# Kernel optimization log

Measured on AMD Instinct MI355X. Metric: run time of the kernel, lower is better.

The kernel has to match this reference:

```python
import jax, jax.numpy as jnp
import numpy as np

DEPTH = 6
IN_DIM = 768
NODE_HIDDEN = 16
LEAF_HIDDEN = 128
OUT_DIM = 768
BATCH = 4096
N_NODES = 2 ** DEPTH - 1   # 63 gating MLPs (heap/BFS order, root first)
N_LEAVES = 2 ** DEPTH      # 64 leaf MLPs


def setup_inputs() -> dict:
    key = jax.random.key(0)
    ks = jax.random.split(key, 5)
    def winit(k, shape, fan_in):
        return jax.random.normal(k, shape, jnp.float32) * (1.0 / np.sqrt(fan_in))
    return {
        "x": jax.random.normal(ks[0], (BATCH, IN_DIM), jnp.float32),
        "node_w1": winit(ks[1], (N_NODES, IN_DIM, NODE_HIDDEN), IN_DIM),
        "node_b1": jnp.zeros((N_NODES, NODE_HIDDEN), jnp.float32),
        "node_w2": winit(ks[2], (N_NODES, NODE_HIDDEN, 1), NODE_HIDDEN),
        "node_b2": jnp.zeros((N_NODES, 1), jnp.float32),
        "leaf_w1": winit(ks[3], (N_LEAVES, IN_DIM, LEAF_HIDDEN), IN_DIM),
        "leaf_b1": jnp.zeros((N_LEAVES, LEAF_HIDDEN), jnp.float32),
        "leaf_w2": winit(ks[4], (N_LEAVES, LEAF_HIDDEN, OUT_DIM), LEAF_HIDDEN),
        "leaf_b2": jnp.zeros((N_LEAVES, OUT_DIM), jnp.float32),
    }


def reference(x, node_w1, node_b1, node_w2, node_b2,
              leaf_w1, leaf_b1, leaf_w2, leaf_b2):
    """Training-mode (soft-gating) FFF tree, fully batched over all nodes/leaves.

    Equivalent to the recursive torch forward with training=True and the
    stochastic output-swap disabled (swap is a training-noise trick).
    """
    B = x.shape[0]
    # All node gates in one pass: c[b, n] = sigmoid(W2 @ relu(W1 @ x + b1) + b2)
    hn = jax.nn.relu(jnp.einsum('bi,nih->bnh', x, node_w1) + node_b1)
    c = jax.nn.sigmoid(jnp.einsum('bnh,nho->bno', hn, node_w2) + node_b2)[..., 0]  # [B, N_NODES]
    # All leaf MLPs in one pass (identity out activation)
    hl = jax.nn.relu(jnp.einsum('bi,lih->blh', x, leaf_w1) + leaf_b1)             # [B, L, LEAF_HIDDEN]
    y = jnp.einsum('blh,lho->blo', hl, leaf_w2) + leaf_b2                         # [B, L, OUT]
    # Leaf mixture weights: product of c (left) / (1-c) (right) along root->leaf path.
    # Heap index idx has children 2*idx, 2*idx+1; gate c weights the LEFT child.
    w = jnp.ones((B, 1), x.dtype)
    for lvl in range(DEPTH):
        g = c[:, 2 ** lvl - 1: 2 ** (lvl + 1) - 1]        # gates at this level, [B, 2^lvl]
        w = jnp.stack([w * g, w * (1.0 - g)], axis=-1).reshape(B, 2 ** (lvl + 1))
    return jnp.einsum('bl,blo->bo', w, y)                 # [B, OUT]
```

## Files before the change

kernel.cpp:

```cpp
#include <hip/hip_runtime.h>
#include <stdint.h>
#include <stddef.h>

typedef __attribute__((ext_vector_type(8))) short short8;
typedef __attribute__((ext_vector_type(4))) float f32x4;
typedef __attribute__((ext_vector_type(4))) short short4v;

__device__ __forceinline__ short f2bf(float f) {
  unsigned u = __builtin_bit_cast(unsigned, f);
  u = (u + 0x7fffu + ((u >> 16) & 1u)) >> 16;
  return (short)u;
}

__device__ __forceinline__ void gload16(const void* g, void* l) {
  __builtin_amdgcn_global_load_lds(
      (const __attribute__((address_space(1))) unsigned int*)g,
      (__attribute__((address_space(3))) unsigned int*)l, 16, 0, 0);
}


__global__ __launch_bounds__(256)
void cvt_misc_k(const float* __restrict__ x, const float* __restrict__ nw1,
                const float* __restrict__ lb2, short* __restrict__ xb,
                short* __restrict__ BTn, short* __restrict__ BT2) {
  const int bx = blockIdx.x;
  if (bx < 3072) {
    const int i = bx * 256 + threadIdx.x;
    const float4 v = ((const float4*)x)[i];
    short4v o;
    o.x = f2bf(v.x); o.y = f2bf(v.y); o.z = f2bf(v.z); o.w = f2bf(v.w);
    *(short4v*)(xb + (size_t)i * 4) = o;
  } else if (bx < 6144) {
    const int idx = (bx - 3072) * 256 + threadIdx.x;
    const int i = idx % 768;
    const int nh = idx / 768;
    float v = 0.f;
    if (nh < 1008) v = nw1[((size_t)(nh >> 4) * 768 + i) * 16 + (nh & 15)];
    BTn[idx] = f2bf(v);
  } else {
    const int idx = (bx - 6144) * 256 + threadIdx.x;
    const int o = idx >> 6, l = idx & 63;
    BT2[(size_t)o * 8256 + 8192 + l] = f2bf(lb2[(size_t)l * 768 + o]);
  }
}

__global__ __launch_bounds__(256, 4)
void node_cvt_k(const short* __restrict__ xb, const short* __restrict__ BTn,
                float* __restrict__ hn, const float* __restrict__ lw1,
                const float* __restrict__ lw2, short* __restrict__ BT1,
                short* __restrict__ BT2) {
  __shared__ char sh[24576];
  const int tid = threadIdx.x;
  if (blockIdx.x < 512) {
    constexpr int ABYTES = 64 * 128;
    const int lane = tid & 63, wid = tid >> 6;
    const int wm = wid >> 1, wn = wid & 1;
    const int sid = (blockIdx.x & 7) * 64 + (blockIdx.x >> 3);
    const int xg = sid % 8, yg = sid / 8;
    const int m0 = yg * 64, n0 = xg * 128;
    f32x4 acc[2][4];
    const f32x4 zero = {0.f, 0.f, 0.f, 0.f};
#pragma unroll
    for (int i = 0; i < 2; ++i)
#pragma unroll
      for (int j = 0; j < 4; ++j) acc[i][j] = zero;
    for (int ki = 0; ki < 12; ++ki) {
      const int k0 = ki * 64;
      __syncthreads();
#pragma unroll
      for (int s = 0; s < 6; ++s) {
        const int off = s * 4096 + tid * 16;
        const short* src;
        if (off < ABYTES) {
          const int r = off >> 7;
          const int cs = ((off >> 4) & 7) ^ (r & 7);
          src = xb + (size_t)(m0 + r) * 768 + k0 + cs * 8;
        } else {
          const int o2 = off - ABYTES;
          const int r = o2 >> 7;
          const int cs = ((o2 >> 4) & 7) ^ (r & 7);
          src = BTn + (size_t)(n0 + r) * 768 + k0 + cs * 8;
        }
        gload16(src, sh + off);
      }
      __syncthreads();
#pragma unroll
      for (int kk = 0; kk < 2; ++kk) {
        const int chunk = kk * 4 + (lane >> 4);
        short8 af[2], bfr[4];
#pragma unroll
        for (int i = 0; i < 2; ++i) {
          const int row = wm * 32 + i * 16 + (lane & 15);
          af[i] = *(const short8*)(sh + row * 128 + ((chunk ^ (row & 7)) << 4));
        }
#pragma unroll
        for (int j = 0; j < 4; ++j) {
          const int row = wn * 64 + j * 16 + (lane & 15);
          bfr[j] = *(const short8*)(sh + ABYTES + row * 128 + ((chunk ^ (row & 7)) << 4));
        }
#pragma unroll
        for (int i = 0; i < 2; ++i)
#pragma unroll
          for (int j = 0; j < 4; ++j)
            acc[i][j] = __builtin_amdgcn_mfma_f32_16x16x32_bf16(af[i], bfr[j], acc[i][j], 0, 0, 0);
      }
    }
    const int row_base = m0 + wm * 32 + (lane >> 4) * 4;
    const int col_base = n0 + wn * 64 + (lane & 15);
#pragma unroll
    for (int i = 0; i < 2; ++i)
#pragma unroll
      for (int j = 0; j < 4; ++j)
#pragma unroll
        for (int r = 0; r < 4; ++r)
          hn[(size_t)(row_base + i * 16 + r) * 1024 + col_base + j * 16] = acc[i][j][r];
  } else {
    float (*tile)[65] = (float(*)[65])sh;
    const int cb = blockIdx.x - 512;
    const int z = cb / 24, rem = cb % 24;
    const int by = rem / 12, bxx = rem % 12;
    const int h0 = by * 64, i0 = bxx * 64;
    if (z < 64) {
      const int l = z;
#pragma unroll
      for (int t = 0; t < 16; ++t) {
        const int e = t * 256 + tid;
        const int ii = e >> 6, hh = e & 63;
        tile[ii][hh] = lw1[(size_t)l * 98304 + (size_t)(i0 + ii) * 128 + (h0 + hh)];
      }
      __syncthreads();
#pragma unroll
      for (int t = 0; t < 16; ++t) {
        const int e = t * 256 + tid;
        const int hh = e >> 6, ii = e & 63;
        BT1[(size_t)(l * 128 + h0 + hh) * 768 + i0 + ii] = f2bf(tile[ii][hh]);
      }
    } else {
      const int l = z - 64;
      const int o0 = i0;
#pragma unroll
      for (int t = 0; t < 16; ++t) {
        const int e = t * 256 + tid;
        const int hh = e >> 6, oo = e & 63;
        tile[hh][oo] = lw2[(size_t)l * 98304 + (size_t)(h0 + hh) * 768 + (o0 + oo)];
      }
      __syncthreads();
#pragma unroll
      for (int t = 0; t < 16; ++t) {
        const int e = t * 256 + tid;
        const int oo = e >> 6, hh = e & 63;
        BT2[(size_t)(o0 + oo) * 8256 + l * 128 + h0 + hh] = f2bf(tile[hh][oo]);
      }
    }
  }
}

__global__ __launch_bounds__(256)
void gates_k(const float* __restrict__ hn, const float* __restrict__ nb1,
             const float* __restrict__ nw2, const float* __restrict__ nb2,
             float* __restrict__ wgt, short* __restrict__ hs) {
  const int b = blockIdx.x * 4 + (threadIdx.x >> 6);
  const int lane = threadIdx.x & 63;
  float c = 0.f;
  if (lane < 63) {
    float s = nb2[lane];
    const float* h = hn + (size_t)b * 1024 + lane * 16;
#pragma unroll
    for (int j = 0; j < 16; ++j) {
      float v = fmaxf(h[j] + nb1[lane * 16 + j], 0.f);
      s += v * nw2[lane * 16 + j];
    }
    c = 1.f / (1.f + expf(-s));
  }
  float w = 1.f;
#pragma unroll
  for (int lvl = 0; lvl < 6; ++lvl) {
    const int idx = (1 << lvl) - 1 + (lane >> (6 - lvl));
    const float g = __shfl(c, idx, 64);
    w *= ((lane >> (5 - lvl)) & 1) ? (1.f - g) : g;
  }
  wgt[(size_t)b * 64 + lane] = w;
  hs[(size_t)b * 8256 + 8192 + lane] = f2bf(w);
}

__global__ __launch_bounds__(512, 2)
void gemm8p(const short* __restrict__ A, const short* __restrict__ B,
            short* __restrict__ C, int KT, int lda, int ldb, int ldc,
            int nx, const float* __restrict__ bias, const float* __restrict__ wgt) {
  constexpr int ABYTES = 256 * 128;
  constexpr int TILEB = 2 * ABYTES;
  __shared__ char lds[2 * TILEB];

  const int tid = threadIdx.x, lane = tid & 63, wid = tid >> 6;
  const int wm = wid >> 2, wn = wid & 3;

  const int cpx = gridDim.x >> 3;
  const int sid = (blockIdx.x & 7) * cpx + (blockIdx.x >> 3);
  const int xg = sid % nx, yg = sid / nx;
  const int m0 = yg * 256, n0 = xg * 256;

  f32x4 acc[8][4];
  const f32x4 zero = {0.f, 0.f, 0.f, 0.f};
#pragma unroll
  for (int i = 0; i < 8; ++i)
#pragma unroll
    for (int j = 0; j < 4; ++j) acc[i][j] = zero;

  auto STG = [&](int buf, int mat, int h, int kt) {
    const int k0 = kt * 64;
    char* dst = lds + buf * TILEB + mat * ABYTES + h * 16384;
    const short* base = mat ? B : A;
    const int ld = mat ? ldb : lda;
    const int r0 = (mat ? n0 : m0) + h * 128;
#pragma unroll
    for (int s = 0; s < 2; ++s) {
      const int off = s * 8192 + tid * 16;
      const int r = off >> 7;
      const int cs = ((off >> 4) & 7) ^ (r & 7);
      gload16(base + (size_t)(r0 + r) * ld + k0 + cs * 8, dst + off);
    }
  };

  short8 bfrag[4][2];
  auto RD_B = [&](int buf) {
    const char* bB = lds + buf * TILEB + ABYTES;
#pragma unroll
    for (int j = 0; j < 4; ++j)
#pragma unroll
      for (int kk = 0; kk < 2; ++kk) {
        const int row = wn * 64 + j * 16 + (lane & 15);
        const int chunk = kk * 4 + (lane >> 4);
        bfrag[j][kk] = *(const short8*)(bB + row * 128 + ((chunk ^ (row & 7)) << 4));
      }
  };

  auto PH = [&](int buf, int q, bool rdB, int vm, auto&& stages) {
    if (rdB) RD_B(buf);
    const char* bA = lds + buf * TILEB;
    short8 af[2][2];
#pragma unroll
    for (int i = 0; i < 2; ++i)
#pragma unroll
      for (int kk = 0; kk < 2; ++kk) {
        const int row = wm * 128 + q * 32 + i * 16 + (lane & 15);
        const int chunk = kk * 4 + (lane >> 4);
        af[i][kk] = *(const short8*)(bA + row * 128 + ((chunk ^ (row & 7)) << 4));
      }
    stages();
    if (vm == 4) asm volatile("s_waitcnt vmcnt(4)" ::: "memory");
    else if (vm == 0) asm volatile("s_waitcnt vmcnt(0)" ::: "memory");
    __builtin_amdgcn_s_barrier();
    __builtin_amdgcn_s_setprio(1);
#pragma unroll
    for (int kk = 0; kk < 2; ++kk)
#pragma unroll
      for (int i = 0; i < 2; ++i)
#pragma unroll
        for (int j = 0; j < 4; ++j)
          acc[q * 2 + i][j] =
              __builtin_amdgcn_mfma_f32_16x16x32_bf16(af[i][kk], bfrag[j][kk], acc[q * 2 + i][j], 0, 0, 0);
    __builtin_amdgcn_s_setprio(0);
    __builtin_amdgcn_s_barrier();
  };

  STG(0, 0, 0, 0); STG(0, 0, 1, 0); STG(0, 1, 0, 0); STG(0, 1, 1, 0);
  STG(1, 1, 0, 1); STG(1, 1, 1, 1);
  asm volatile("s_waitcnt vmcnt(4)" ::: "memory");
  __builtin_amdgcn_s_barrier();

  const int iters = KT >> 1;
  for (int it = 0; it < iters; ++it) {
    const int t0 = it * 2;
    const bool last = (it == iters - 1);
    PH(0, 0, true, -1, [&] { if (t0 + 1 < KT) STG(1, 0, 0, t0 + 1); });
    PH(0, 1, false, -1, [&] {
      if (t0 + 1 < KT) STG(1, 0, 1, t0 + 1);
      if (t0 + 2 < KT) STG(0, 1, 0, t0 + 2);
    });
    PH(0, 2, false, -1, [&] { if (t0 + 2 < KT) STG(0, 1, 1, t0 + 2); });
    PH(0, 3, false, last ? 0 : 4, [] {});
    PH(1, 0, true, -1, [&] { if (t0 + 2 < KT) STG(0, 0, 0, t0 + 2); });
    PH(1, 1, false, -1, [&] { if (t0 + 2 < KT) STG(0, 0, 1, t0 + 2); });
    PH(1, 2, false, -1, [&] { if (t0 + 3 < KT) STG(1, 1, 0, t0 + 3); });
    PH(1, 3, false, last ? -1 : 4, [&] { if (t0 + 3 < KT) STG(1, 1, 1, t0 + 3); });
  }

#pragma unroll
  for (int mi = 0; mi < 8; ++mi) {
    const int row_base = m0 + wm * 128 + mi * 16 + (lane >> 4) * 4;
#pragma unroll
    for (int j = 0; j < 4; ++j) {
      const int col = n0 + wn * 64 + j * 16 + (lane & 15);
      const int leaf = col >> 7;
      const float b = bias[col];
#pragma unroll
      for (int r = 0; r < 4; ++r) {
        const int row = row_base + r;
        const float v = fmaxf(acc[mi][j][r] + b, 0.f) * wgt[(size_t)row * 64 + leaf];
        C[(size_t)row * ldc + col] = f2bf(v);
      }
    }
  }
}

__global__ __launch_bounds__(256, 3)
void gemm2k(const short* __restrict__ A, const short* __restrict__ B,
            float* __restrict__ Out, float* __restrict__ P1,
            float* __restrict__ P2, float* __restrict__ P3,
            int KT, int ks, int lda, int ldb, int ldc, int nx, int ny) {
  constexpr int BM = 128;
  constexpr int ABYTES = BM * 128;
  constexpr int BBYTES = 128 * 128;
  constexpr int FM = BM / 32;
  constexpr int NLOAD = (ABYTES + BBYTES) / (256 * 16);
  __shared__ char lds[ABYTES + BBYTES];

  const int tid = threadIdx.x, lane = tid & 63, wid = tid >> 6;
  const int wm = wid >> 1, wn = wid & 1;

  const int cpx = gridDim.x >> 3;
  const int sid = (blockIdx.x & 7) * cpx + (blockIdx.x >> 3);
  const int xg = sid % nx;
  const int t1 = sid / nx;
  const int yg = t1 % ny;
  const int z = t1 / ny;
  const int m0 = yg * BM, n0 = xg * 128;
  const int kt0 = z * ks;
  const int ktn = min(ks, KT - kt0);

  f32x4 acc[FM][4];
  const f32x4 zero = {0.f, 0.f, 0.f, 0.f};
#pragma unroll
  for (int i = 0; i < FM; ++i)
#pragma unroll
    for (int j = 0; j < 4; ++j) acc[i][j] = zero;

  for (int ki = 0; ki < ktn; ++ki) {
    const int k0 = (kt0 + ki) * 64;
    __syncthreads();
#pragma unroll
    for (int s = 0; s < NLOAD; ++s) {
      const int off = s * 4096 + tid * 16;
      const short* src;
      if (off < ABYTES) {
        const int r = off >> 7;
        const int cs = ((off >> 4) & 7) ^ (r & 7);
        src = A + (size_t)(m0 + r) * lda + k0 + cs * 8;
      } else {
        const int o2 = off - ABYTES;
        const int r = o2 >> 7;
        const int cs = ((o2 >> 4) & 7) ^ (r & 7);
        src = B + (size_t)(n0 + r) * ldb + k0 + cs * 8;
      }
      gload16(src, lds + off);
    }
    __syncthreads();

    const char* ldsA = lds;
    const char* ldsB = lds + ABYTES;
#pragma unroll
    for (int kk = 0; kk < 2; ++kk) {
      const int chunk = kk * 4 + (lane >> 4);
      short8 af[FM], bfr[4];
#pragma unroll
      for (int i = 0; i < FM; ++i) {
        const int row = wm * (BM / 2) + i * 16 + (lane & 15);
        af[i] = *(const short8*)(ldsA + row * 128 + ((chunk ^ (row & 7)) << 4));
      }
#pragma unroll
      for (int j = 0; j < 4; ++j) {
        const int row = wn * 64 + j * 16 + (lane & 15);
        bfr[j] = *(const short8*)(ldsB + row * 128 + ((chunk ^ (row & 7)) << 4));
      }
      __builtin_amdgcn_s_setprio(1);
#pragma unroll
      for (int i = 0; i < FM; ++i)
#pragma unroll
        for (int j = 0; j < 4; ++j)
          acc[i][j] = __builtin_amdgcn_mfma_f32_16x16x32_bf16(af[i], bfr[j], acc[i][j], 0, 0, 0);
      __builtin_amdgcn_s_setprio(0);
    }
  }

  const int row_base = m0 + wm * (BM / 2) + (lane >> 4) * 4;
  const int col_base = n0 + wn * 64 + (lane & 15);
  float* C = (z == 0) ? Out : (z == 1 ? P1 : (z == 2 ? P2 : P3));
#pragma unroll
  for (int i = 0; i < FM; ++i)
#pragma unroll
    for (int j = 0; j < 4; ++j) {
      const int col = col_base + j * 16;
#pragma unroll
      for (int r = 0; r < 4; ++r) {
        const int row = row_base + i * 16 + r;
        C[(size_t)row * ldc + col] = acc[i][j][r];
      }
    }
}

__global__ __launch_bounds__(256)
void reduce_k(float* __restrict__ out, const float* __restrict__ p1,
              const float* __restrict__ p2, const float* __restrict__ p3) {
  const int i = blockIdx.x * 256 + threadIdx.x;
  f32x4 a = ((const f32x4*)out)[i];
  f32x4 b = ((const f32x4*)p1)[i];
  f32x4 c = ((const f32x4*)p2)[i];
  f32x4 d = ((const f32x4*)p3)[i];
  ((f32x4*)out)[i] = (a + b) + (c + d);
}


extern "C" void kernel_launch(void* const* d_in, const int* in_sizes, int n_in,
                              void* d_out, int out_size, void* d_ws, size_t ws_size,
                              hipStream_t stream) {
  const float* x   = (const float*)d_in[0];
  const float* nw1 = (const float*)d_in[1];
  const float* nb1 = (const float*)d_in[2];
  const float* nw2 = (const float*)d_in[3];
  const float* nb2 = (const float*)d_in[4];
  const float* lw1 = (const float*)d_in[5];
  const float* lb1 = (const float*)d_in[6];
  const float* lw2 = (const float*)d_in[7];
  const float* lb2 = (const float*)d_in[8];

  char* ws = (char*)d_ws;
  short* xb  = (short*)(ws + 0);
  short* BT1 = (short*)(ws + 6291456);
  short* BTn = (short*)(ws + 18874368);
  float* hn  = (float*)(ws + 20447232);
  float* wgt = (float*)(ws + 37224448);
  short* BT2 = (short*)(ws + 38273024);
  short* hs  = (short*)(ws + 50954240);
  float* p1  = (float*)(ws + 0);
  float* p2  = (float*)(ws + 12582912);
  float* p3  = (float*)(ws + 25165824);

  cvt_misc_k<<<6336, 256, 0, stream>>>(x, nw1, lb2, xb, BTn, BT2);
  node_cvt_k<<<3584, 256, 0, stream>>>(xb, BTn, hn, lw1, lw2, BT1, BT2);

  gates_k<<<1024, 256, 0, stream>>>(hn, nb1, nw2, nb2, wgt, hs);

  gemm8p<<<512, 512, 0, stream>>>(xb, BT1, hs, 12, 768, 768, 8256, 32, lb1, wgt);

  gemm2k<<<768, 256, 0, stream>>>(hs, BT2, (float*)d_out, p1, p2, p3,
                                  129, 33, 8256, 8256, 768, 6, 32);
  reduce_k<<<3072, 256, 0, stream>>>((float*)d_out, p1, p2, p3);
}
```

Measured before the change: 169.2 us.

## Reuse 256x256 pipelined GEMM for second leaf GEMM with split-K

```diff
diff --git a/kernel.cpp b/kernel.cpp
--- a/kernel.cpp
+++ b/kernel.cpp
@@ -183,10 +183,15 @@
   hs[(size_t)b * 8256 + 8192 + lane] = f2bf(w);
 }
 
+template <int EPI>
 __global__ __launch_bounds__(512, 2)
-void gemm8p(const short* __restrict__ A, const short* __restrict__ B,
-            short* __restrict__ C, int KT, int lda, int ldb, int ldc,
-            int nx, const float* __restrict__ bias, const float* __restrict__ wgt) {
+void gemm8x(const short* __restrict__ A, const short* __restrict__ B,
+            void* __restrict__ C0, float* __restrict__ P1, float* __restrict__ P2,
+            float* __restrict__ P3, const float* __restrict__ bias,
+            const float* __restrict__ wgt) {
+  constexpr int LDA = EPI ? 768 : 8256;
+  constexpr int LDB = EPI ? 768 : 8256;
+  constexpr int LDC = EPI ? 8256 : 768;
   constexpr int ABYTES = 256 * 128;
   constexpr int TILEB = 2 * ABYTES;
   __shared__ char lds[2 * TILEB];
@@ -194,9 +199,20 @@
   const int tid = threadIdx.x, lane = tid & 63, wid = tid >> 6;
   const int wm = wid >> 2, wn = wid & 3;
 
-  const int cpx = gridDim.x >> 3;
-  const int sid = (blockIdx.x & 7) * cpx + (blockIdx.x >> 3);
-  const int xg = sid % nx, yg = sid / nx;
+  const int c = blockIdx.x & 7, ii = blockIdx.x >> 3;
+  int xg, yg, kt0, ktn, zz;
+  if constexpr (EPI == 1) {
+    xg = ((c & 3) << 3) + (ii & 7);
+    yg = ((c >> 2) << 3) + (ii >> 3);
+    kt0 = 0; ktn = 12; zz = 0;
+  } else {
+    xg = ii % 3;
+    const int yz = c * 8 + ii / 3;
+    yg = yz & 15;
+    zz = yz >> 4;
+    kt0 = zz * 32;
+    ktn = (zz == 3) ? 33 : 32;
+  }
   const int m0 = yg * 256, n0 = xg * 256;
 
   f32x4 acc[8][4];
@@ -210,7 +226,7 @@
     const int k0 = kt * 64;
     char* dst = lds + buf * TILEB + mat * ABYTES + h * 16384;
     const short* base = mat ? B : A;
-    const int ld = mat ? ldb : lda;
+    const int ld = mat ? LDB : LDA;
     const int r0 = (mat ? n0 : m0) + h * 128;
 #pragma unroll
     for (int s = 0; s < 2; ++s) {
@@ -263,139 +279,91 @@
     __builtin_amdgcn_s_barrier();
   };
 
-  STG(0, 0, 0, 0); STG(0, 0, 1, 0); STG(0, 1, 0, 0); STG(0, 1, 1, 0);
-  STG(1, 1, 0, 1); STG(1, 1, 1, 1);
+  STG(0, 0, 0, kt0); STG(0, 0, 1, kt0); STG(0, 1, 0, kt0); STG(0, 1, 1, kt0);
+  STG(1, 1, 0, kt0 + 1); STG(1, 1, 1, kt0 + 1);
   asm volatile("s_waitcnt vmcnt(4)" ::: "memory");
   __builtin_amdgcn_s_barrier();
 
-  const int iters = KT >> 1;
+  const int iters = ktn >> 1;
   for (int it = 0; it < iters; ++it) {
     const int t0 = it * 2;
-    const bool last = (it == iters - 1);
-    PH(0, 0, true, -1, [&] { if (t0 + 1 < KT) STG(1, 0, 0, t0 + 1); });
+    const bool lastp = (it == iters - 1) && !(ktn & 1);
+    const bool t2 = t0 + 2 < ktn, t3 = t0 + 3 < ktn;
+    PH(0, 0, true, -1, [&] { STG(1, 0, 0, kt0 + t0 + 1); });
     PH(0, 1, false, -1, [&] {
-      if (t0 + 1 < KT) STG(1, 0, 1, t0 + 1);
-      if (t0 + 2 < KT) STG(0, 1, 0, t0 + 2);
+      STG(1, 0, 1, kt0 + t0 + 1);
+      if (t2) STG(0, 1, 0, kt0 + t0 + 2);
     });
-    PH(0, 2, false, -1, [&] { if (t0 + 2 < KT) STG(0, 1, 1, t0 + 2); });
-    PH(0, 3, false, last ? 0 : 4, [] {});
-    PH(1, 0, true, -1, [&] { if (t0 + 2 < KT) STG(0, 0, 0, t0 + 2); });
-    PH(1, 1, false, -1, [&] { if (t0 + 2 < KT) STG(0, 0, 1, t0 + 2); });
-    PH(1, 2, false, -1, [&] { if (t0 + 3 < KT) STG(1, 1, 0, t0 + 3); });
-    PH(1, 3, false, last ? -1 : 4, [&] { if (t0 + 3 < KT) STG(1, 1, 1, t0 + 3); });
-  }
-
-#pragma unroll
-  for (int mi = 0; mi < 8; ++mi) {
-    const int row_base = m0 + wm * 128 + mi * 16 + (lane >> 4) * 4;
-#pragma unroll
-    for (int j = 0; j < 4; ++j) {
-      const int col = n0 + wn * 64 + j * 16 + (lane & 15);
-      const int leaf = col >> 7;
-      const float b = bias[col];
-#pragma unroll
-      for (int r = 0; r < 4; ++r) {
-        const int row = row_base + r;
-        const float v = fmaxf(acc[mi][j][r] + b, 0.f) * wgt[(size_t)row * 64 + leaf];
-        C[(size_t)row * ldc + col] = f2bf(v);
-      }
-    }
-  }
-}
-
-__global__ __launch_bounds__(256, 3)
-void gemm2k(const short* __restrict__ A, const short* __restrict__ B,
-            float* __restrict__ Out, float* __restrict__ P1,
-            float* __restrict__ P2, float* __restrict__ P3,
-            int KT, int ks, int lda, int ldb, int ldc, int nx, int ny) {
-  constexpr int BM = 128;
-  constexpr int ABYTES = BM * 128;
-  constexpr int BBYTES = 128 * 128;
-  constexpr int FM = BM / 32;
-  constexpr int NLOAD = (ABYTES + BBYTES) / (256 * 16);
-  __shared__ char lds[ABYTES + BBYTES];
-
-  const int tid = threadIdx.x, lane = tid & 63, wid = tid >> 6;
-  const int wm = wid >> 1, wn = wid & 1;
-
-  const int cpx = gridDim.x >> 3;
-  const int sid = (blockIdx.x & 7) * cpx + (blockIdx.x >> 3);
-  const int xg = sid % nx;
-  const int t1 = sid / nx;
-  const int yg = t1 % ny;
-  const int z = t1 / ny;
-  const int m0 = yg * BM, n0 = xg * 128;
-  const int kt0 = z * ks;
-  const int ktn = min(ks, KT - kt0);
-
-  f32x4 acc[FM][4];
-  const f32x4 zero = {0.f, 0.f, 0.f, 0.f};
-#pragma unroll
-  for (int i = 0; i < FM; ++i)
-#pragma unroll
-    for (int j = 0; j < 4; ++j) acc[i][j] = zero;
-
-  for (int ki = 0; ki < ktn; ++ki) {
-    const int k0 = (kt0 + ki) * 64;
-    __syncthreads();
-#pragma unroll
-    for (int s = 0; s < NLOAD; ++s) {
-      const int off = s * 4096 + tid * 16;
-      const short* src;
-      if (off < ABYTES) {
-        const int r = off >> 7;
-        const int cs = ((off >> 4) & 7) ^ (r & 7);
-        src = A + (size_t)(m0 + r) * lda + k0 + cs * 8;
-      } else {
-        const int o2 = off - ABYTES;
-        const int r = o2 >> 7;
-        const int cs = ((o2 >> 4) & 7) ^ (r & 7);
-        src = B + (size_t)(n0 + r) * ldb + k0 + cs * 8;
-      }
-      gload16(src, lds + off);
-    }
-    __syncthreads();
-
-    const char* ldsA = lds;
-    const char* ldsB = lds + ABYTES;
-#pragma unroll
-    for (int kk = 0; kk < 2; ++kk) {
-      const int chunk = kk * 4 + (lane >> 4);
-      short8 af[FM], bfr[4];
-#pragma unroll
-      for (int i = 0; i < FM; ++i) {
-        const int row = wm * (BM / 2) + i * 16 + (lane & 15);
-        af[i] = *(const short8*)(ldsA + row * 128 + ((chunk ^ (row & 7)) << 4));
-      }
+    PH(0, 2, false, -1, [&] { if (t2) STG(0, 1, 1, kt0 + t0 + 2); });
+    PH(0, 3, false, lastp ? 0 : 4, [] {});
+    PH(1, 0, true, -1, [&] { if (t2) STG(0, 0, 0, kt0 + t0 + 2); });
+    PH(1, 1, false, -1, [&] { if (t2) STG(0, 0, 1, kt0 + t0 + 2); });
+    PH(1, 2, false, -1, [&] { if (t3) STG(1, 1, 0, kt0 + t0 + 3); });
+    PH(1, 3, false, lastp ? -1 : 4, [&] { if (t3) STG(1, 1, 1, kt0 + t0 + 3); });
+  }
+  if (ktn & 1) {
+    asm volatile("s_waitcnt vmcnt(0)" ::: "memory");
+    __builtin_amdgcn_s_barrier();
+    RD_B(0);
+    const char* bA = lds;
+#pragma unroll
+    for (int q = 0; q < 4; ++q) {
+      short8 af[2][2];
+#pragma unroll
+      for (int i = 0; i < 2; ++i)
+#pragma unroll
+        for (int kk = 0; kk < 2; ++kk) {
+          const int row = wm * 128 + q * 32 + i * 16 + (lane & 15);
+          const int chunk = kk * 4 + (lane >> 4);
+          af[i][kk] = *(const short8*)(bA + row * 128 + ((chunk ^ (row & 7)) << 4));
+        }
+      __builtin_amdgcn_s_setprio(1);
+#pragma unroll
+      for (int kk = 0; kk < 2; ++kk)
+#pragma unroll
+        for (int i = 0; i < 2; ++i)
+#pragma unroll
+          for (int j = 0; j < 4; ++j)
+            acc[q * 2 + i][j] =
+                __builtin_amdgcn_mfma_f32_16x16x32_bf16(af[i][kk], bfrag[j][kk], acc[q * 2 + i][j], 0, 0, 0);
+      __builtin_amdgcn_s_setprio(0);
+    }
+  }
+
+  if constexpr (EPI == 1) {
+    short* C = (short*)C0;
+#pragma unroll
+    for (int mi = 0; mi < 8; ++mi) {
+      const int row_base = m0 + wm * 128 + mi * 16 + (lane >> 4) * 4;
 #pragma unroll
       for (int j = 0; j < 4; ++j) {
-        const int row = wn * 64 + j * 16 + (lane & 15);
-        bfr[j] = *(const short8*)(ldsB + row * 128 + ((chunk ^ (row & 7)) << 4));
-      }
-      __builtin_amdgcn_s_setprio(1);
-#pragma unroll
-      for (int i = 0; i < FM; ++i)
-#pragma unroll
-        for (int j = 0; j < 4; ++j)
-          acc[i][j] = __builtin_amdgcn_mfma_f32_16x16x32_bf16(af[i], bfr[j], acc[i][j], 0, 0, 0);
-      __builtin_amdgcn_s_setprio(0);
-    }
-  }
-
-  const int row_base = m0 + wm * (BM / 2) + (lane >> 4) * 4;
-  const int col_base = n0 + wn * 64 + (lane & 15);
-  float* C = (z == 0) ? Out : (z == 1 ? P1 : (z == 2 ? P2 : P3));
-#pragma unroll
-  for (int i = 0; i < FM; ++i)
-#pragma unroll
-    for (int j = 0; j < 4; ++j) {
-      const int col = col_base + j * 16;
-#pragma unroll
-      for (int r = 0; r < 4; ++r) {
-        const int row = row_base + i * 16 + r;
-        C[(size_t)row * ldc + col] = acc[i][j][r];
-      }
-    }
+        const int col = n0 + wn * 64 + j * 16 + (lane & 15);
+        const int leaf = col >> 7;
+        const float b = bias[col];
+#pragma unroll
+        for (int r = 0; r < 4; ++r) {
+          const int row = row_base + r;
+          const float v = fmaxf(acc[mi][j][r] + b, 0.f) * wgt[(size_t)row * 64 + leaf];
+          C[(size_t)row * LDC + col] = f2bf(v);
+        }
+      }
+    }
+  } else {
+    float* C = (zz == 0) ? (float*)C0 : (zz == 1 ? P1 : (zz == 2 ? P2 : P3));
+#pragma unroll
+    for (int mi = 0; mi < 8; ++mi) {
+      const int row_base = m0 + wm * 128 + mi * 16 + (lane >> 4) * 4;
+#pragma unroll
+      for (int j = 0; j < 4; ++j) {
+        const int col = n0 + wn * 64 + j * 16 + (lane & 15);
+#pragma unroll
+        for (int r = 0; r < 4; ++r) {
+          const int row = row_base + r;
+          C[(size_t)row * LDC + col] = acc[mi][j][r];
+        }
+      }
+    }
+  }
 }
 
 __global__ __launch_bounds__(256)
@@ -440,9 +408,11 @@
 
   gates_k<<<1024, 256, 0, stream>>>(hn, nb1, nw2, nb2, wgt, hs);
 
-  gemm8p<<<512, 512, 0, stream>>>(xb, BT1, hs, 12, 768, 768, 8256, 32, lb1, wgt);
-
-  gemm2k<<<768, 256, 0, stream>>>(hs, BT2, (float*)d_out, p1, p2, p3,
-                                  129, 33, 8256, 8256, 768, 6, 32);
+  gemm8x<1><<<512, 512, 0, stream>>>(xb, BT1, hs, nullptr, nullptr, nullptr,
+                                     lb1, wgt);
+
+  gemm8x<0><<<192, 512, 0, stream>>>(hs, BT2, d_out, p1, p2, p3,
+                                     nullptr, nullptr);
+
   reduce_k<<<3072, 256, 0, stream>>>((float*)d_out, p1, p2, p3);
 }
```

Result: faster. 161.1 us (-4.8%).
